# Performance work log

Hardware: AMD Instinct MI355X
Metric: run time of the kernel (lower is better)

The kernel has to match this reference:

```python
import jax, jax.numpy as jnp
import numpy as np

ALPHA = 0.99
EPS = 1e-14


def setup_inputs() -> dict:
    key = jax.random.key(0)
    B, C, T, F = 16, 1, 2000, 481
    x = jax.random.normal(key, (B, C, T, F, 2), dtype=jnp.float32)
    # unit_norm_init: linearly decaying initial norm state over freq bins
    init_state = jnp.linspace(0.001, 0.0001, F, dtype=jnp.float32).reshape(1, 1, F, 1)
    return {"x": x, "init_state": init_state}


def reference(x, init_state):
    # x: [B, C, T, F, 2] (real/imag), init_state: [1, 1, F, 1]
    B, C, T, F, _ = x.shape
    # complex magnitude per (b,c,t,f), clamped for stability: [B, C, T, F, 1]
    x_abs = jnp.sqrt(jnp.maximum(jnp.sum(x * x, axis=-1, keepdims=True), EPS))
    # scan over time: state = (1-alpha)*|x_t| + alpha*state
    xs = jnp.moveaxis(x_abs, 2, 0)  # [T, B, C, F, 1]
    s0 = jnp.broadcast_to(init_state, (B, C, F, 1)).astype(x.dtype)

    def step(s, xt):
        s = xt * (1.0 - ALPHA) + s * ALPHA
        return s, s

    _, states = jax.lax.scan(step, s0, xs)  # [T, B, C, F, 1]
    states = jnp.moveaxis(states, 0, 2)  # [B, C, T, F, 1]
    return x / jnp.sqrt(states)
```

## Files before the change

### kernel.cpp

```cpp
#include <hip/hip_runtime.h>


#define ALPHA_F 0.99f
#define OMA_F   0.01f
#define EPS_F   1e-14f

typedef float f32x4 __attribute__((ext_vector_type(4)));

constexpr int Bn = 16;
constexpr int Tn = 2000;
constexpr int Fn = 481;
constexpr int NC = 100;
constexpr int L  = Tn / NC;
constexpr int ST = 4;
constexpr int NST = L / ST;
constexpr int RF  = 2 * Fn;
constexpr int SF4 = ST * RF / 4;
constexpr int TL3 = SF4 - 3 * 256;
constexpr int MT = 25;
#define ALPHA_L 0.817906938f

__global__ __launch_bounds__(256) void eun_pass1(
    const float* __restrict__ x, float* __restrict__ part) {
  __shared__ f32x4 lds[2][SF4];
  const int tid = threadIdx.x;
  const int c = blockIdx.x, b = blockIdx.y;

  const size_t base_f = ((size_t)b * Tn + (size_t)c * L) * RF;
  const f32x4* xb = (const f32x4*)(x + base_f);

  f32x4 v[4];
#pragma unroll
  for (int j = 0; j < 3; ++j) v[j] = xb[tid + 256 * j];
  if (tid < TL3) v[3] = xb[tid + 256 * 3];
#pragma unroll
  for (int j = 0; j < 3; ++j) lds[0][tid + 256 * j] = v[j];
  if (tid < TL3) lds[0][tid + 256 * 3] = v[3];
  __syncthreads();

  const int f1 = tid, f2 = tid + 256;
  float s1 = 0.f, s2 = 0.f;
  int cur = 0;
  for (int st = 0; st < NST; ++st) {
    if (st + 1 < NST) {
      const f32x4* sb = xb + (size_t)(st + 1) * SF4;
#pragma unroll
      for (int j = 0; j < 3; ++j) v[j] = sb[tid + 256 * j];
      if (tid < TL3) v[3] = sb[tid + 256 * 3];
    }
    const float2* l2 = (const float2*)lds[cur];
#pragma unroll
    for (int r = 0; r < ST; ++r) {
      float2 a = l2[r * Fn + f1];
      float m = sqrtf(fmaxf(fmaf(a.x, a.x, a.y * a.y), EPS_F));
      s1 = fmaf(ALPHA_F, s1, OMA_F * m);
      if (f2 < Fn) {
        float2 q = l2[r * Fn + f2];
        float m2 = sqrtf(fmaxf(fmaf(q.x, q.x, q.y * q.y), EPS_F));
        s2 = fmaf(ALPHA_F, s2, OMA_F * m2);
      }
    }
    if (st + 1 < NST) {
#pragma unroll
      for (int j = 0; j < 3; ++j) lds[cur ^ 1][tid + 256 * j] = v[j];
      if (tid < TL3) lds[cur ^ 1][tid + 256 * 3] = v[3];
    }
    __syncthreads();
    cur ^= 1;
  }
  float* pp = part + ((size_t)b * NC + c) * Fn;
  pp[f1] = s1;
  if (f2 < Fn) pp[f2] = s2;
}

__global__ __launch_bounds__(256) void eun_mid(
    const float* __restrict__ init_state, float* __restrict__ part) {
  const int f = blockIdx.x * blockDim.x + threadIdx.x;
  if (f >= Fn) return;
  const int b = blockIdx.y;
  float* pp = part + (size_t)b * NC * Fn + f;
  float s = init_state[f];
  for (int c0 = 0; c0 < NC; c0 += MT) {
    float p[MT];
#pragma unroll
    for (int k = 0; k < MT; ++k) p[k] = pp[(size_t)(c0 + k) * Fn];
#pragma unroll
    for (int k = 0; k < MT; ++k) {
      pp[(size_t)(c0 + k) * Fn] = s;
      s = fmaf(s, ALPHA_L, p[k]);
    }
  }
}

__global__ __launch_bounds__(256) void eun_pass2(
    const float* __restrict__ x, const float* __restrict__ start,
    float* __restrict__ out) {
  __shared__ f32x4 lds[2][SF4];
  const int tid = threadIdx.x;
  const int c = blockIdx.x, b = blockIdx.y;

  const size_t base_f = ((size_t)b * Tn + (size_t)c * L) * RF;
  const int f1 = tid, f2 = tid + 256;
  const bool a2 = (f2 < Fn);

  float s1 = start[((size_t)b * NC + c) * Fn + f1];
  float s2 = a2 ? start[((size_t)b * NC + c) * Fn + f2] : 0.f;

  const float* xp1 = x + base_f + (size_t)f1 * 2;
  const float* xp2 = x + base_f + (size_t)f2 * 2;

  float2 av[ST], qv[ST], an[ST], qn[ST];
#pragma unroll
  for (int r = 0; r < ST; ++r) {
    av[r] = *(const float2*)(xp1 + (size_t)r * RF);
    if (a2) qv[r] = *(const float2*)(xp2 + (size_t)r * RF);
  }

  int cur = 0;
  for (int st = 0; st < NST; ++st) {
    if (st + 1 < NST) {
      const float* p1 = xp1 + (size_t)(st + 1) * ST * RF;
      const float* p2 = xp2 + (size_t)(st + 1) * ST * RF;
#pragma unroll
      for (int r = 0; r < ST; ++r) {
        an[r] = *(const float2*)(p1 + (size_t)r * RF);
        if (a2) qn[r] = *(const float2*)(p2 + (size_t)r * RF);
      }
    }
    float2* l2 = (float2*)lds[cur];
#pragma unroll
    for (int r = 0; r < ST; ++r) {
      float m = sqrtf(fmaxf(fmaf(av[r].x, av[r].x, av[r].y * av[r].y), EPS_F));
      s1 = fmaf(ALPHA_F, s1, OMA_F * m);
      float inv1 = rsqrtf(s1);
      l2[r * Fn + f1] = make_float2(av[r].x * inv1, av[r].y * inv1);
      if (a2) {
        float m2 = sqrtf(fmaxf(fmaf(qv[r].x, qv[r].x, qv[r].y * qv[r].y), EPS_F));
        s2 = fmaf(ALPHA_F, s2, OMA_F * m2);
        float inv2 = rsqrtf(s2);
        l2[r * Fn + f2] = make_float2(qv[r].x * inv2, qv[r].y * inv2);
      }
    }
    __syncthreads();
    f32x4* ob = (f32x4*)(out + base_f) + (size_t)st * SF4;
    const f32x4* ls = (const f32x4*)lds[cur];
#pragma unroll
    for (int j = 0; j < 3; ++j) {
      f32x4 o = ls[tid + 256 * j];
      __builtin_nontemporal_store(o, ob + tid + 256 * j);
    }
    if (tid < TL3) {
      f32x4 o = ls[tid + 256 * 3];
      __builtin_nontemporal_store(o, ob + tid + 256 * 3);
    }
#pragma unroll
    for (int r = 0; r < ST; ++r) { av[r] = an[r]; qv[r] = qn[r]; }
    cur ^= 1;
  }
}

extern "C" void kernel_launch(void* const* d_in, const int* in_sizes, int n_in,
                              void* d_out, int out_size, void* d_ws, size_t ws_size,
                              hipStream_t stream) {
  const float* x    = (const float*)d_in[0];
  const float* init = (const float*)d_in[1];
  float* out        = (float*)d_out;
  float* part       = (float*)d_ws;

  dim3 grid(NC, Bn);
  eun_pass1<<<grid, dim3(256), 0, stream>>>(x, part);
  eun_mid<<<dim3((Fn + 255) / 256, Bn), dim3(256), 0, stream>>>(init, part);
  eun_pass2<<<grid, dim3(256), 0, stream>>>(x, part, out);
}
```

Before: 241.6 us.

## Replace pass1 sequential chunk scan with weighted sum via LDS atomics

Pass 1 no longer walks each chunk's time steps in order. Each chunk's end state is instead computed as a weighted sum of magnitudes with precomputed weights 0.01*alpha^(L-1-t), so the whole chunk can be read linearly with float4 loads, without the LDS double-buffer staging. The per-frequency sums are gathered with shared-memory float atomicAdd. This removes the serial dependency and the barriers, but adds LDS atomic contention, an integer divide per element, and a different float summation order.

```diff
diff --git a/kernel.cpp b/kernel.cpp
--- a/kernel.cpp
+++ b/kernel.cpp
@@ -12,65 +12,63 @@
 constexpr int Fn = 481;
 constexpr int NC = 100;
 constexpr int L  = Tn / NC;
+constexpr int RF = 2 * Fn;
+constexpr int NF4 = L * RF / 4;
+constexpr int FULL = NF4 / 256;
+constexpr int REM  = NF4 - FULL * 256;
 constexpr int ST = 4;
 constexpr int NST = L / ST;
-constexpr int RF  = 2 * Fn;
 constexpr int SF4 = ST * RF / 4;
 constexpr int TL3 = SF4 - 3 * 256;
 constexpr int MT = 25;
 #define ALPHA_L 0.817906938f
 
-__global__ __launch_bounds__(256) void eun_pass1(
+__global__ __launch_bounds__(256) void eun_pass1lin(
     const float* __restrict__ x, float* __restrict__ part) {
-  __shared__ f32x4 lds[2][SF4];
+  __shared__ float B_lds[Fn];
+  __shared__ float w_lds[L];
   const int tid = threadIdx.x;
   const int c = blockIdx.x, b = blockIdx.y;
 
-  const size_t base_f = ((size_t)b * Tn + (size_t)c * L) * RF;
-  const f32x4* xb = (const f32x4*)(x + base_f);
-
-  f32x4 v[4];
-#pragma unroll
-  for (int j = 0; j < 3; ++j) v[j] = xb[tid + 256 * j];
-  if (tid < TL3) v[3] = xb[tid + 256 * 3];
-#pragma unroll
-  for (int j = 0; j < 3; ++j) lds[0][tid + 256 * j] = v[j];
-  if (tid < TL3) lds[0][tid + 256 * 3] = v[3];
+  B_lds[tid] = 0.f;
+  if (tid < Fn - 256) B_lds[tid + 256] = 0.f;
+  if (tid < L) w_lds[tid] = OMA_F * powf(ALPHA_F, (float)(L - 1 - tid));
   __syncthreads();
 
-  const int f1 = tid, f2 = tid + 256;
-  float s1 = 0.f, s2 = 0.f;
-  int cur = 0;
-  for (int st = 0; st < NST; ++st) {
-    if (st + 1 < NST) {
-      const f32x4* sb = xb + (size_t)(st + 1) * SF4;
-#pragma unroll
-      for (int j = 0; j < 3; ++j) v[j] = sb[tid + 256 * j];
-      if (tid < TL3) v[3] = sb[tid + 256 * 3];
-    }
-    const float2* l2 = (const float2*)lds[cur];
-#pragma unroll
-    for (int r = 0; r < ST; ++r) {
-      float2 a = l2[r * Fn + f1];
-      float m = sqrtf(fmaxf(fmaf(a.x, a.x, a.y * a.y), EPS_F));
-      s1 = fmaf(ALPHA_F, s1, OMA_F * m);
-      if (f2 < Fn) {
-        float2 q = l2[r * Fn + f2];
-        float m2 = sqrtf(fmaxf(fmaf(q.x, q.x, q.y * q.y), EPS_F));
-        s2 = fmaf(ALPHA_F, s2, OMA_F * m2);
-      }
-    }
-    if (st + 1 < NST) {
-#pragma unroll
-      for (int j = 0; j < 3; ++j) lds[cur ^ 1][tid + 256 * j] = v[j];
-      if (tid < TL3) lds[cur ^ 1][tid + 256 * 3] = v[3];
-    }
-    __syncthreads();
-    cur ^= 1;
+  const f32x4* xb = (const f32x4*)(x + ((size_t)b * Tn + (size_t)c * L) * RF);
+
+#pragma unroll 6
+  for (int k = 0; k < FULL; ++k) {
+    const int i = tid + 256 * k;
+    f32x4 v = xb[i];
+    const int g0 = 2 * i;
+    const int t0 = g0 / Fn;
+    const int f0 = g0 - t0 * Fn;
+    float m0 = sqrtf(fmaxf(fmaf(v.x, v.x, v.y * v.y), EPS_F));
+    atomicAdd(&B_lds[f0], w_lds[t0] * m0);
+    int f1 = f0 + 1, t1 = t0;
+    if (f1 == Fn) { f1 = 0; ++t1; }
+    float m1 = sqrtf(fmaxf(fmaf(v.z, v.z, v.w * v.w), EPS_F));
+    atomicAdd(&B_lds[f1], w_lds[t1] * m1);
   }
+  if (tid < REM) {
+    const int i = tid + 256 * FULL;
+    f32x4 v = xb[i];
+    const int g0 = 2 * i;
+    const int t0 = g0 / Fn;
+    const int f0 = g0 - t0 * Fn;
+    float m0 = sqrtf(fmaxf(fmaf(v.x, v.x, v.y * v.y), EPS_F));
+    atomicAdd(&B_lds[f0], w_lds[t0] * m0);
+    int f1 = f0 + 1, t1 = t0;
+    if (f1 == Fn) { f1 = 0; ++t1; }
+    float m1 = sqrtf(fmaxf(fmaf(v.z, v.z, v.w * v.w), EPS_F));
+    atomicAdd(&B_lds[f1], w_lds[t1] * m1);
+  }
+  __syncthreads();
+
   float* pp = part + ((size_t)b * NC + c) * Fn;
-  pp[f1] = s1;
-  if (f2 < Fn) pp[f2] = s2;
+  pp[tid] = B_lds[tid];
+  if (tid < Fn - 256) pp[tid + 256] = B_lds[tid + 256];
 }
 
 __global__ __launch_bounds__(256) void eun_mid(
@@ -168,7 +166,7 @@
   float* part       = (float*)d_ws;
 
   dim3 grid(NC, Bn);
-  eun_pass1<<<grid, dim3(256), 0, stream>>>(x, part);
+  eun_pass1lin<<<grid, dim3(256), 0, stream>>>(x, part);
   eun_mid<<<dim3((Fn + 255) / 256, Bn), dim3(256), 0, stream>>>(init, part);
   eun_pass2<<<grid, dim3(256), 0, stream>>>(x, part, out);
 }
```

After: 279.8 us. +15.8%, slower.
